# Kernel tuning notes

Hardware: AMD Instinct MI355X
Metric: run time of the kernel (lower is better)

## Reference

```python
import jax, jax.numpy as jnp
import numpy as np

N = 65536   # base nodes
M = 65536   # union local nodes
E = 1048576 # base edges
EL = 1048576 # local edges
K = 131072  # membership entries
F = 128     # in_channels
H = 128     # hidden_dim
L = 2       # num_layers
OUT = 2
ALPHA = 0.9


def setup_inputs() -> dict:
    key = jax.random.key(0)
    ks = jax.random.split(key, 16)
    s = 1.0 / np.sqrt(H)
    return {
        "x": jax.random.normal(ks[0], (N, F), jnp.float32),
        "edge_index": jax.random.randint(ks[1], (2, E), 0, N, jnp.int64 if jax.config.jax_enable_x64 else jnp.int32),
        "edge_weight": jax.random.uniform(ks[2], (E,), jnp.float32),
        "local_x0": jax.random.normal(ks[3], (M, F), jnp.float32),
        "copy2orig": jax.random.randint(ks[4], (M,), 0, N),
        "local_adj_index": jax.random.randint(ks[5], (2, EL), 0, M),
        "local_adj_value": jax.random.uniform(ks[6], (EL,), jnp.float32),
        "memb_idx": jax.random.randint(ks[7], (K,), 0, M),
        "memb_gid": jax.random.randint(ks[8], (K,), 0, 64),
        "B": 64,
        "Wb_in": jax.random.normal(ks[9], (F, H), jnp.float32) * s,
        "bb_in": jnp.zeros((H,), jnp.float32),
        "Wl_in": jax.random.normal(ks[10], (F, H), jnp.float32) * s,
        "bl_in": jnp.zeros((H,), jnp.float32),
        "W_base": jax.random.normal(ks[11], (L, H, H), jnp.float32) * s,
        "b_base": jnp.zeros((L, H), jnp.float32),
        "W_local": jax.random.normal(ks[12], (L, H, H), jnp.float32) * s,
        "b_local": jnp.zeros((L, H), jnp.float32),
        "Wp": jax.random.normal(ks[13], (H, OUT), jnp.float32) * s,
        "bp": jnp.zeros((OUT,), jnp.float32),
    }


def reference(x, edge_index, edge_weight, local_x0, copy2orig, local_adj_index,
              local_adj_value, memb_idx, memb_gid, B, Wb_in, bb_in, Wl_in, bl_in,
              W_base, b_base, W_local, b_local, Wp, bp):
    n = x.shape[0]
    m = local_x0.shape[0]
    # input projections (dropout is identity in eval mode)
    base_x = jax.nn.relu(x @ Wb_in + bb_in)
    local_x = jax.nn.relu(local_x0 @ Wl_in + bl_in)
    src, dst = edge_index[0], edge_index[1]
    lsrc, ldst = local_adj_index[0], local_adj_index[1]
    for l in range(W_base.shape[0]):
        # base graph propagation: normalized-adjacency spmm then linear+relu
        base_agg = jax.ops.segment_sum(base_x[src] * edge_weight[:, None], dst, num_segments=n)
        base_x = jax.nn.relu(base_agg @ W_base[l] + b_base[l])
        # local union-graph propagation + alpha-mix with base features via copy2orig
        local_agg = jax.ops.segment_sum(local_x[lsrc] * local_adj_value[:, None], ldst, num_segments=m)
        mix = ALPHA * local_agg + (1.0 - ALPHA) * base_x[copy2orig]
        local_x = jax.nn.relu(mix @ W_local[l] + b_local[l])
    # scatter-mean pooling by membership (fused sum + count)
    sub = jax.ops.segment_sum(local_x[memb_idx], memb_gid, num_segments=B)
    cnt = jax.ops.segment_sum(jnp.ones((memb_gid.shape[0], 1), local_x.dtype), memb_gid, num_segments=B)
    sub = sub / jnp.maximum(cnt, 1.0)
    return sub @ Wp + bp
```

## Files before the change

### kernel.cpp

```cpp
#include <hip/hip_runtime.h>

typedef __attribute__((ext_vector_type(8))) short bfrag;
typedef __attribute__((ext_vector_type(4))) float ffrag;

__device__ __forceinline__ ushort f2bf(float f) {
    union { float f; unsigned u; } v{f};
    unsigned r = v.u + 0x7fff + ((v.u >> 16) & 1);
    return (ushort)(r >> 16);
}
__device__ __forceinline__ float bf2f(ushort u) {
    union { unsigned u; float f; } v{(unsigned)u << 16};
    return v.f;
}
__device__ __forceinline__ float bflo(unsigned u) {
    union { unsigned u; float f; } v{u << 16};
    return v.f;
}
__device__ __forceinline__ float bfhi(unsigned u) {
    union { unsigned u; float f; } v{u & 0xffff0000u};
    return v.f;
}


__global__ __launch_bounds__(256) void zero_all(int* __restrict__ a, int* __restrict__ b,
                                                int* __restrict__ c, int* __restrict__ d) {
    int i = blockIdx.x * 256 + threadIdx.x;
    if (i < 256) { a[i] = 0; b[i] = 0; }
    if (i < 64) c[i] = 0;
    if (i < 64 * 128) d[i] = 0;
}


__global__ __launch_bounds__(256) void bhist(const int* __restrict__ dst, int* __restrict__ bcount) {
    __shared__ int h[256];
    const int t = threadIdx.x;
    h[t] = 0;
    __syncthreads();
    const int base = blockIdx.x * 4096;
#pragma unroll
    for (int u = 0; u < 16; ++u)
        atomicAdd(&h[((unsigned)dst[base + u * 256 + t]) >> 8], 1);
    __syncthreads();
    atomicAdd(&bcount[t], h[t]);
}

__global__ __launch_bounds__(256) void bscan(const int* __restrict__ bcount, int* __restrict__ bstart,
                                             int* __restrict__ bcursor) {
    __shared__ int s[256];
    const int t = threadIdx.x;
    int c = bcount[t];
    s[t] = c;
    __syncthreads();
    for (int o = 1; o < 256; o <<= 1) {
        int add = (t >= o) ? s[t - o] : 0;
        __syncthreads();
        s[t] += add;
        __syncthreads();
    }
    int excl = s[t] - c;
    bstart[t] = excl;
    bcursor[t] = excl;
    if (t == 255) bstart[256] = s[t];
}

#define CH 4096

__global__ __launch_bounds__(1024) void bucket1(const int* __restrict__ src, const int* __restrict__ dst,
                                                const float* __restrict__ w, int* __restrict__ bcursor,
                                                int2* __restrict__ staged) {
    __shared__ int cnt_s[256], base_l[256], base_g[256], cur[256];
    __shared__ int2 stage[CH];
    __shared__ unsigned char bb[CH];
    const int t = threadIdx.x;
    const int base = blockIdx.x * CH;
    if (t < 256) cnt_s[t] = 0;
    __syncthreads();
#pragma unroll
    for (int u = 0; u < CH / 1024; ++u) {
        int b = ((unsigned)dst[base + u * 1024 + t]) >> 8;
        atomicAdd(&cnt_s[b], 1);
    }
    __syncthreads();
    int v = 0;
    if (t < 256) { v = cnt_s[t]; base_l[t] = v; }
    __syncthreads();
    for (int o = 1; o < 256; o <<= 1) {
        int add = 0;
        if (t < 256 && t >= o) add = base_l[t - o];
        __syncthreads();
        if (t < 256) base_l[t] += add;
        __syncthreads();
    }
    if (t < 256) {
        int excl = base_l[t] - v;
        base_l[t] = excl;
        cur[t] = excl;
        base_g[t] = atomicAdd(&bcursor[t], v);
    }
    __syncthreads();
#pragma unroll
    for (int u = 0; u < CH / 1024; ++u) {
        int e = base + u * 1024 + t;
        int d = dst[e];
        int b = ((unsigned)d) >> 8;
        int p = atomicAdd(&cur[b], 1);
        stage[p] = make_int2((src[e] & 0xffff) | ((d & 255) << 16), __float_as_int(w[e]));
        bb[p] = (unsigned char)b;
    }
    __syncthreads();
    for (int i = t; i < CH; i += 1024) {
        int b = bb[i];
        staged[base_g[b] + (i - base_l[b])] = stage[i];
    }
}

__global__ __launch_bounds__(1024) void bucket2n(const int* __restrict__ bstart, const int2* __restrict__ staged,
                                                 int* __restrict__ start, int2* __restrict__ edges) {
    __shared__ int cnt[256], excl[256], cur[256];
    const int t = threadIdx.x;
    const int b = blockIdx.x;
    if (t < 256) cnt[t] = 0;
    __syncthreads();
    const int s0 = bstart[b];
    const int s1 = bstart[b + 1];
    for (int i = s0 + t; i < s1; i += 1024) {
        int dl = (staged[i].x >> 16) & 0xff;
        atomicAdd(&cnt[dl], 1);
    }
    __syncthreads();
    int v = 0;
    if (t < 256) { v = cnt[t]; excl[t] = v; }
    __syncthreads();
    for (int o = 1; o < 256; o <<= 1) {
        int add = 0;
        if (t < 256 && t >= o) add = excl[t - o];
        __syncthreads();
        if (t < 256) excl[t] += add;
        __syncthreads();
    }
    if (t < 256) {
        int e = excl[t] - v;
        cur[t] = e;
        start[b * 256 + t] = s0 + e;
        if (b == 255 && t == 255) start[256 * 256] = s1;
    }
    __syncthreads();
    for (int i = s0 + t; i < s1; i += 1024) {
        int2 se = staged[i];
        int dl = (se.x >> 16) & 0xff;
        int p = s0 + atomicAdd(&cur[dl], 1);
        edges[p] = make_int2(se.x & 0xffff, se.y);
    }
}


__global__ __launch_bounds__(256) void wprep(const float* __restrict__ Wb_in, const float* __restrict__ Wl_in,
                                             const float* __restrict__ W_base, const float* __restrict__ W_local,
                                             ushort* __restrict__ out) {
    int idx = blockIdx.x * 256 + threadIdx.x;
    int mat = idx >> 14;
    int i = idx & 16383;
    int nn = i >> 7, kk = i & 127;
    const float* src;
    switch (mat) {
        case 0: src = Wb_in; break;
        case 1: src = Wl_in; break;
        case 2: src = W_base; break;
        case 3: src = W_base + 16384; break;
        case 4: src = W_local; break;
        default: src = W_local + 16384; break;
    }
    out[(size_t)mat * 16384 + i] = f2bf(src[kk * 128 + nn]);
}

#define ASTRIDE 136


template <bool A_F32, bool MIX>
__global__ __launch_bounds__(256) void gemm_mfma(const void* __restrict__ Ap, const ushort* __restrict__ A2,
                                                 const int* __restrict__ ridx,
                                                 const ushort* __restrict__ Wt, const float* __restrict__ bias,
                                                 ushort* __restrict__ Y) {
    __shared__ ushort As[64 * ASTRIDE];
    __shared__ ushort Bs[128 * ASTRIDE];
    const int tid = threadIdx.x;
    const int r0 = blockIdx.x * 64;

    if (A_F32) {
        const float* A = (const float*)Ap;
#pragma unroll
        for (int p = 0; p < 8; ++p) {
            int c = p * 256 + tid;
            int row = c >> 5, o4 = (c & 31) * 4;
            float4 v = *(const float4*)(A + (size_t)(r0 + row) * 128 + o4);
            ushort4 u;
            u.x = f2bf(v.x); u.y = f2bf(v.y); u.z = f2bf(v.z); u.w = f2bf(v.w);
            *(ushort4*)&As[row * ASTRIDE + o4] = u;
        }
    } else {
        const ushort* A = (const ushort*)Ap;
#pragma unroll
        for (int p = 0; p < 4; ++p) {
            int c = p * 256 + tid;
            int row = c >> 4, o8 = (c & 15) * 8;
            uint4 v = *(const uint4*)(A + (size_t)(r0 + row) * 128 + o8);
            if (MIX) {
                int rr = ridx[r0 + row];
                uint4 v2 = *(const uint4*)(A2 + (size_t)rr * 128 + o8);
                uint4 o;
                float x0, x1;
                x0 = 0.9f * bflo(v.x) + 0.1f * bflo(v2.x);
                x1 = 0.9f * bfhi(v.x) + 0.1f * bfhi(v2.x);
                o.x = (unsigned)f2bf(x0) | ((unsigned)f2bf(x1) << 16);
                x0 = 0.9f * bflo(v.y) + 0.1f * bflo(v2.y);
                x1 = 0.9f * bfhi(v.y) + 0.1f * bfhi(v2.y);
                o.y = (unsigned)f2bf(x0) | ((unsigned)f2bf(x1) << 16);
                x0 = 0.9f * bflo(v.z) + 0.1f * bflo(v2.z);
                x1 = 0.9f * bfhi(v.z) + 0.1f * bfhi(v2.z);
                o.z = (unsigned)f2bf(x0) | ((unsigned)f2bf(x1) << 16);
                x0 = 0.9f * bflo(v.w) + 0.1f * bflo(v2.w);
                x1 = 0.9f * bfhi(v.w) + 0.1f * bfhi(v2.w);
                o.w = (unsigned)f2bf(x0) | ((unsigned)f2bf(x1) << 16);
                v = o;
            }
            *(uint4*)&As[row * ASTRIDE + o8] = v;
        }
    }
#pragma unroll
    for (int p = 0; p < 8; ++p) {
        int c = p * 256 + tid;
        int n = c >> 4, o8 = (c & 15) * 8;
        *(uint4*)&Bs[n * ASTRIDE + o8] = *(const uint4*)(Wt + n * 128 + o8);
    }
    __syncthreads();

    const int lane = tid & 63;
    const int w = tid >> 6;
    const int wm = (w & 1) * 32;
    const int wn = (w >> 1) * 64;
    const int q = lane >> 4;
    const int l16 = lane & 15;

    ffrag acc[2][4];
#pragma unroll
    for (int mt = 0; mt < 2; ++mt)
#pragma unroll
        for (int nt = 0; nt < 4; ++nt) acc[mt][nt] = (ffrag){0.f, 0.f, 0.f, 0.f};

#pragma unroll
    for (int kc = 0; kc < 4; ++kc) {
        bfrag a[2], b[4];
#pragma unroll
        for (int mt = 0; mt < 2; ++mt)
            a[mt] = *(const bfrag*)&As[(wm + mt * 16 + l16) * ASTRIDE + kc * 32 + q * 8];
#pragma unroll
        for (int nt = 0; nt < 4; ++nt)
            b[nt] = *(const bfrag*)&Bs[(wn + nt * 16 + l16) * ASTRIDE + kc * 32 + q * 8];
#pragma unroll
        for (int mt = 0; mt < 2; ++mt)
#pragma unroll
            for (int nt = 0; nt < 4; ++nt)
                acc[mt][nt] = __builtin_amdgcn_mfma_f32_16x16x32_bf16(a[mt], b[nt], acc[mt][nt], 0, 0, 0);
    }

    float bias_v[4];
#pragma unroll
    for (int nt = 0; nt < 4; ++nt) bias_v[nt] = bias[wn + nt * 16 + l16];
#pragma unroll
    for (int mt = 0; mt < 2; ++mt)
#pragma unroll
        for (int nt = 0; nt < 4; ++nt)
#pragma unroll
            for (int r = 0; r < 4; ++r) {
                int row = r0 + wm + mt * 16 + q * 4 + r;
                int col = wn + nt * 16 + l16;
                float v = fmaxf(acc[mt][nt][r] + bias_v[nt], 0.f);
                Y[(size_t)row * 128 + col] = f2bf(v);
            }
}


__global__ __launch_bounds__(256) void spmm_bf16(const int* __restrict__ start, const int2* __restrict__ edges,
                                                 const ushort* __restrict__ X, ushort* __restrict__ Y, int n) {
    int node = (blockIdx.x * 256 + threadIdx.x) >> 5;
    int lane = threadIdx.x & 31;
    if (node >= n) return;
    int s0 = start[node];
    int s1 = start[node + 1];
    const int f = lane * 4;
    float a0 = 0.f, a1 = 0.f, a2 = 0.f, a3 = 0.f;
    int e = s0;
    for (; e + 4 <= s1; e += 4) {
        int2 e0 = edges[e + 0], e1 = edges[e + 1], e2 = edges[e + 2], e3 = edges[e + 3];
        float w0 = __int_as_float(e0.y), w1 = __int_as_float(e1.y);
        float w2 = __int_as_float(e2.y), w3 = __int_as_float(e3.y);
        ushort4 v0 = *(const ushort4*)(X + (size_t)e0.x * 128 + f);
        ushort4 v1 = *(const ushort4*)(X + (size_t)e1.x * 128 + f);
        ushort4 v2 = *(const ushort4*)(X + (size_t)e2.x * 128 + f);
        ushort4 v3 = *(const ushort4*)(X + (size_t)e3.x * 128 + f);
        a0 += w0 * bf2f(v0.x) + w1 * bf2f(v1.x) + w2 * bf2f(v2.x) + w3 * bf2f(v3.x);
        a1 += w0 * bf2f(v0.y) + w1 * bf2f(v1.y) + w2 * bf2f(v2.y) + w3 * bf2f(v3.y);
        a2 += w0 * bf2f(v0.z) + w1 * bf2f(v1.z) + w2 * bf2f(v2.z) + w3 * bf2f(v3.z);
        a3 += w0 * bf2f(v0.w) + w1 * bf2f(v1.w) + w2 * bf2f(v2.w) + w3 * bf2f(v3.w);
    }
    for (; e < s1; ++e) {
        int2 ee = edges[e];
        float w = __int_as_float(ee.y);
        ushort4 v = *(const ushort4*)(X + (size_t)ee.x * 128 + f);
        a0 += w * bf2f(v.x);
        a1 += w * bf2f(v.y);
        a2 += w * bf2f(v.z);
        a3 += w * bf2f(v.w);
    }
    ushort4 o;
    o.x = f2bf(a0);
    o.y = f2bf(a1);
    o.z = f2bf(a2);
    o.w = f2bf(a3);
    *(ushort4*)(Y + (size_t)node * 128 + f) = o;
}


__global__ __launch_bounds__(256) void pool_hist(const int* __restrict__ memb_gid, int* __restrict__ gcount) {
    __shared__ int h[64];
    int t = threadIdx.x;
    if (t < 64) h[t] = 0;
    __syncthreads();
    int base = blockIdx.x * 1024;
#pragma unroll
    for (int u = 0; u < 4; ++u) atomicAdd(&h[memb_gid[base + u * 256 + t]], 1);
    __syncthreads();
    if (t < 64) atomicAdd(&gcount[t], h[t]);
}

__global__ __launch_bounds__(64) void pool_scan(const int* __restrict__ gcount, int* __restrict__ gstart,
                                                int* __restrict__ cursor) {
    __shared__ int s[64];
    int t = threadIdx.x;
    int c = gcount[t];
    s[t] = c;
    __syncthreads();
    int acc = 0;
    for (int j = 0; j < 64; ++j)
        if (j < t) acc += s[j];
    gstart[t] = acc;
    cursor[t] = acc;
    if (t == 63) gstart[64] = acc + c;
}

__global__ __launch_bounds__(256) void pool_scatter(const int* __restrict__ memb_idx,
                                                    const int* __restrict__ memb_gid,
                                                    int* __restrict__ cursor, int* __restrict__ sorted_idx) {
    __shared__ int lhist[64];
    __shared__ int lbase[64];
    __shared__ int loff[1024];
    int t = threadIdx.x;
    if (t < 64) lhist[t] = 0;
    __syncthreads();
    int base = blockIdx.x * 1024;
    int g[4], ix[4];
#pragma unroll
    for (int u = 0; u < 4; ++u) {
        int e = base + u * 256 + t;
        g[u] = memb_gid[e];
        ix[u] = memb_idx[e];
        loff[u * 256 + t] = atomicAdd(&lhist[g[u]], 1);
    }
    __syncthreads();
    if (t < 64) lbase[t] = atomicAdd(&cursor[t], lhist[t]);
    __syncthreads();
#pragma unroll
    for (int u = 0; u < 4; ++u) {
        int pos = lbase[g[u]] + loff[u * 256 + t];
        sorted_idx[pos] = ix[u];
    }
}

__global__ __launch_bounds__(256) void pool_accum(const int* __restrict__ gstart, const int* __restrict__ sorted_idx,
                                                  const ushort* __restrict__ X, float* __restrict__ gsum) {
    const int g = blockIdx.x >> 5;
    const int sgm = blockIdx.x & 31;
    const int gs = gstart[g];
    const int cnt = gstart[g + 1] - gs;
    const int e_begin = gs + ((cnt * sgm) >> 5);
    const int e_end = gs + ((cnt * (sgm + 1)) >> 5);
    const int t = threadIdx.x;
    const int fp = t & 63;
    const int sub = t >> 6;
    float ax = 0.f, ay = 0.f;
#pragma unroll 4
    for (int e = e_begin + sub; e < e_end; e += 4) {
        int idx = sorted_idx[e];
        ushort2 u = *(const ushort2*)(X + (size_t)idx * 128 + fp * 2);
        ax += bf2f(u.x);
        ay += bf2f(u.y);
    }
    __shared__ float sx[256], sy[256];
    sx[t] = ax;
    sy[t] = ay;
    __syncthreads();
    if (t < 64) {
        atomicAdd(&gsum[g * 128 + fp * 2 + 0], sx[t] + sx[t + 64] + sx[t + 128] + sx[t + 192]);
        atomicAdd(&gsum[g * 128 + fp * 2 + 1], sy[t] + sy[t + 64] + sy[t + 128] + sy[t + 192]);
    }
}


__global__ __launch_bounds__(128) void final_kernel(const float* __restrict__ gsum, const int* __restrict__ gcnt,
                                                    const float* __restrict__ Wp, const float* __restrict__ bp,
                                                    float* __restrict__ out) {
    int t = threadIdx.x;
    int g = t >> 1;
    int o = t & 1;
    float inv = 1.f / fmaxf((float)gcnt[g], 1.f);
    float acc = bp[o];
    for (int f = 0; f < 128; ++f) acc += gsum[g * 128 + f] * inv * Wp[f * 2 + o];
    out[g * 2 + o] = acc;
}


extern "C" void kernel_launch(void* const* d_in, const int* in_sizes, int n_in,
                              void* d_out, int out_size, void* d_ws, size_t ws_size,
                              hipStream_t stream) {
    const float* x              = (const float*)d_in[0];
    const int*   edge_index     = (const int*)d_in[1];
    const float* edge_weight    = (const float*)d_in[2];
    const float* local_x0       = (const float*)d_in[3];
    const int*   copy2orig      = (const int*)d_in[4];
    const int*   local_adj_idx  = (const int*)d_in[5];
    const float* local_adj_val  = (const float*)d_in[6];
    const int*   memb_idx       = (const int*)d_in[7];
    const int*   memb_gid       = (const int*)d_in[8];
    const float* Wb_in          = (const float*)d_in[10];
    const float* bb_in          = (const float*)d_in[11];
    const float* Wl_in          = (const float*)d_in[12];
    const float* bl_in          = (const float*)d_in[13];
    const float* W_base         = (const float*)d_in[14];
    const float* b_base         = (const float*)d_in[15];
    const float* W_local        = (const float*)d_in[16];
    const float* b_local        = (const float*)d_in[17];
    const float* Wp             = (const float*)d_in[18];
    const float* bp             = (const float*)d_in[19];
    float* out = (float*)d_out;

    constexpr int N = 65536, M = 65536, E = 1048576, EL = 1048576, K = 131072, H = 128;

    char* wsb = (char*)d_ws;
    size_t off = 0;
    auto alloc = [&](size_t bytes) -> char* {
        char* p = wsb + off;
        off += (bytes + 255) & ~(size_t)255;
        return p;
    };
    int*    bs_start = (int*)alloc((size_t)(N + 1) * 4);
    int2*   bs_edges = (int2*)alloc((size_t)E * 8);
    int2*   bs_stage = (int2*)alloc((size_t)E * 8);
    int*    bs_bcnt  = (int*)alloc(256 * 4);
    int*    bs_bsta  = (int*)alloc(257 * 4);
    int*    bs_bcur  = (int*)alloc(256 * 4);
    int*    ls_start = (int*)alloc((size_t)(M + 1) * 4);
    int2*   ls_edges = (int2*)alloc((size_t)EL * 8);
    int2*   ls_stage = (int2*)alloc((size_t)EL * 8);
    int*    ls_bcnt  = (int*)alloc(256 * 4);
    int*    ls_bsta  = (int*)alloc(257 * 4);
    int*    ls_bcur  = (int*)alloc(256 * 4);
    ushort* bufA     = (ushort*)alloc((size_t)N * H * 2);
    ushort* bufB     = (ushort*)alloc((size_t)M * H * 2);
    ushort* bufC     = (ushort*)alloc((size_t)N * H * 2);
    ushort* bufD     = (ushort*)alloc((size_t)M * H * 2);
    ushort* wt       = (ushort*)alloc((size_t)6 * 16384 * 2);
    int*    p_gcnt   = (int*)alloc(64 * 4);
    int*    p_gstart = (int*)alloc(65 * 4);
    int*    p_cursor = (int*)alloc(64 * 4);
    int*    p_sorted = (int*)alloc((size_t)K * 4);
    float*  pool_sum = (float*)alloc(64 * 128 * 4);

    const int* b_src = edge_index;
    const int* b_dst = edge_index + E;
    const int* l_src = local_adj_idx;
    const int* l_dst = local_adj_idx + EL;

    zero_all<<<32, 256, 0, stream>>>(bs_bcnt, ls_bcnt, p_gcnt, (int*)pool_sum);

    wprep<<<384, 256, 0, stream>>>(Wb_in, Wl_in, W_base, W_local, wt);

    bhist<<<E / 4096, 256, 0, stream>>>(b_dst, bs_bcnt);
    bscan<<<1, 256, 0, stream>>>(bs_bcnt, bs_bsta, bs_bcur);
    bucket1<<<E / CH, 1024, 0, stream>>>(b_src, b_dst, edge_weight, bs_bcur, bs_stage);
    bucket2n<<<256, 1024, 0, stream>>>(bs_bsta, bs_stage, bs_start, bs_edges);

    bhist<<<EL / 4096, 256, 0, stream>>>(l_dst, ls_bcnt);
    bscan<<<1, 256, 0, stream>>>(ls_bcnt, ls_bsta, ls_bcur);
    bucket1<<<EL / CH, 1024, 0, stream>>>(l_src, l_dst, local_adj_val, ls_bcur, ls_stage);
    bucket2n<<<256, 1024, 0, stream>>>(ls_bsta, ls_stage, ls_start, ls_edges);

    pool_hist<<<K / 1024, 256, 0, stream>>>(memb_gid, p_gcnt);
    pool_scan<<<1, 64, 0, stream>>>(p_gcnt, p_gstart, p_cursor);
    pool_scatter<<<K / 1024, 256, 0, stream>>>(memb_idx, memb_gid, p_cursor, p_sorted);

    gemm_mfma<true, false><<<N / 64, 256, 0, stream>>>(x, nullptr, nullptr, wt, bb_in, bufA);
    gemm_mfma<true, false><<<M / 64, 256, 0, stream>>>(local_x0, nullptr, nullptr, wt + 16384, bl_in, bufB);

    for (int l = 0; l < 2; ++l) {
        spmm_bf16<<<N * 32 / 256, 256, 0, stream>>>(bs_start, bs_edges, bufA, bufC, N);
        spmm_bf16<<<M * 32 / 256, 256, 0, stream>>>(ls_start, ls_edges, bufB, bufD, M);
        gemm_mfma<false, false><<<N / 64, 256, 0, stream>>>(bufC, nullptr, nullptr,
                                                            wt + (size_t)(2 + l) * 16384, b_base + (size_t)l * H, bufA);
        gemm_mfma<false, true><<<M / 64, 256, 0, stream>>>(bufD, bufA, copy2orig,
                                                           wt + (size_t)(4 + l) * 16384, b_local + (size_t)l * H, bufB);
    }

    pool_accum<<<64 * 32, 256, 0, stream>>>(p_gstart, p_sorted, bufB, pool_sum);
    final_kernel<<<1, 128, 0, stream>>>(pool_sum, p_gcnt, Wp, bp, out);
}
```

Baseline: 458.3 us.

## Fuse SpMM aggregation with following MFMA GEMM and alpha-mix per layer

Replaces the separate SpMM and GEMM kernels with one kernel per graph that aggregates 64 node rows into shared memory, then runs the MFMA GEMM with bias and ReLU on that tile. The alpha-mix is now applied in fp32 on the aggregate before the bf16 rounding, rather than on rounded bf16 inputs inside the GEMM. Ping-pong buffers avoid read/write aliasing. This removes the intermediate bf16 writes and reads of the aggregated features and two kernel launches per layer. In exchange the weight fragments are read straight from global memory instead of shared memory, and each block serialises 8 node aggregations before the GEMM, which can lower occupancy and latency hiding.

```diff
diff --git a/kernel.cpp b/kernel.cpp
--- a/kernel.cpp
+++ b/kernel.cpp
@@ -176,9 +176,7 @@
 #define ASTRIDE 136
 
 
-template <bool A_F32, bool MIX>
-__global__ __launch_bounds__(256) void gemm_mfma(const void* __restrict__ Ap, const ushort* __restrict__ A2,
-                                                 const int* __restrict__ ridx,
+__global__ __launch_bounds__(256) void gemm_mfma(const float* __restrict__ A,
                                                  const ushort* __restrict__ Wt, const float* __restrict__ bias,
                                                  ushort* __restrict__ Y) {
     __shared__ ushort As[64 * ASTRIDE];
@@ -186,45 +184,14 @@
     const int tid = threadIdx.x;
     const int r0 = blockIdx.x * 64;
 
-    if (A_F32) {
-        const float* A = (const float*)Ap;
-#pragma unroll
-        for (int p = 0; p < 8; ++p) {
-            int c = p * 256 + tid;
-            int row = c >> 5, o4 = (c & 31) * 4;
-            float4 v = *(const float4*)(A + (size_t)(r0 + row) * 128 + o4);
-            ushort4 u;
-            u.x = f2bf(v.x); u.y = f2bf(v.y); u.z = f2bf(v.z); u.w = f2bf(v.w);
-            *(ushort4*)&As[row * ASTRIDE + o4] = u;
-        }
-    } else {
-        const ushort* A = (const ushort*)Ap;
-#pragma unroll
-        for (int p = 0; p < 4; ++p) {
-            int c = p * 256 + tid;
-            int row = c >> 4, o8 = (c & 15) * 8;
-            uint4 v = *(const uint4*)(A + (size_t)(r0 + row) * 128 + o8);
-            if (MIX) {
-                int rr = ridx[r0 + row];
-                uint4 v2 = *(const uint4*)(A2 + (size_t)rr * 128 + o8);
-                uint4 o;
-                float x0, x1;
-                x0 = 0.9f * bflo(v.x) + 0.1f * bflo(v2.x);
-                x1 = 0.9f * bfhi(v.x) + 0.1f * bfhi(v2.x);
-                o.x = (unsigned)f2bf(x0) | ((unsigned)f2bf(x1) << 16);
-                x0 = 0.9f * bflo(v.y) + 0.1f * bflo(v2.y);
-                x1 = 0.9f * bfhi(v.y) + 0.1f * bfhi(v2.y);
-                o.y = (unsigned)f2bf(x0) | ((unsigned)f2bf(x1) << 16);
-                x0 = 0.9f * bflo(v.z) + 0.1f * bflo(v2.z);
-                x1 = 0.9f * bfhi(v.z) + 0.1f * bfhi(v2.z);
-                o.z = (unsigned)f2bf(x0) | ((unsigned)f2bf(x1) << 16);
-                x0 = 0.9f * bflo(v.w) + 0.1f * bflo(v2.w);
-                x1 = 0.9f * bfhi(v.w) + 0.1f * bfhi(v2.w);
-                o.w = (unsigned)f2bf(x0) | ((unsigned)f2bf(x1) << 16);
-                v = o;
-            }
-            *(uint4*)&As[row * ASTRIDE + o8] = v;
-        }
+#pragma unroll
+    for (int p = 0; p < 8; ++p) {
+        int c = p * 256 + tid;
+        int row = c >> 5, o4 = (c & 31) * 4;
+        float4 v = *(const float4*)(A + (size_t)(r0 + row) * 128 + o4);
+        ushort4 u;
+        u.x = f2bf(v.x); u.y = f2bf(v.y); u.z = f2bf(v.z); u.w = f2bf(v.w);
+        *(ushort4*)&As[row * ASTRIDE + o4] = u;
     }
 #pragma unroll
     for (int p = 0; p < 8; ++p) {
@@ -280,44 +247,107 @@
 }
 
 
-__global__ __launch_bounds__(256) void spmm_bf16(const int* __restrict__ start, const int2* __restrict__ edges,
-                                                 const ushort* __restrict__ X, ushort* __restrict__ Y, int n) {
-    int node = (blockIdx.x * 256 + threadIdx.x) >> 5;
-    int lane = threadIdx.x & 31;
-    if (node >= n) return;
-    int s0 = start[node];
-    int s1 = start[node + 1];
-    const int f = lane * 4;
-    float a0 = 0.f, a1 = 0.f, a2 = 0.f, a3 = 0.f;
-    int e = s0;
-    for (; e + 4 <= s1; e += 4) {
-        int2 e0 = edges[e + 0], e1 = edges[e + 1], e2 = edges[e + 2], e3 = edges[e + 3];
-        float w0 = __int_as_float(e0.y), w1 = __int_as_float(e1.y);
-        float w2 = __int_as_float(e2.y), w3 = __int_as_float(e3.y);
-        ushort4 v0 = *(const ushort4*)(X + (size_t)e0.x * 128 + f);
-        ushort4 v1 = *(const ushort4*)(X + (size_t)e1.x * 128 + f);
-        ushort4 v2 = *(const ushort4*)(X + (size_t)e2.x * 128 + f);
-        ushort4 v3 = *(const ushort4*)(X + (size_t)e3.x * 128 + f);
-        a0 += w0 * bf2f(v0.x) + w1 * bf2f(v1.x) + w2 * bf2f(v2.x) + w3 * bf2f(v3.x);
-        a1 += w0 * bf2f(v0.y) + w1 * bf2f(v1.y) + w2 * bf2f(v2.y) + w3 * bf2f(v3.y);
-        a2 += w0 * bf2f(v0.z) + w1 * bf2f(v1.z) + w2 * bf2f(v2.z) + w3 * bf2f(v3.z);
-        a3 += w0 * bf2f(v0.w) + w1 * bf2f(v1.w) + w2 * bf2f(v2.w) + w3 * bf2f(v3.w);
-    }
-    for (; e < s1; ++e) {
-        int2 ee = edges[e];
-        float w = __int_as_float(ee.y);
-        ushort4 v = *(const ushort4*)(X + (size_t)ee.x * 128 + f);
-        a0 += w * bf2f(v.x);
-        a1 += w * bf2f(v.y);
-        a2 += w * bf2f(v.z);
-        a3 += w * bf2f(v.w);
-    }
-    ushort4 o;
-    o.x = f2bf(a0);
-    o.y = f2bf(a1);
-    o.z = f2bf(a2);
-    o.w = f2bf(a3);
-    *(ushort4*)(Y + (size_t)node * 128 + f) = o;
+template <bool MIX>
+__global__ __launch_bounds__(256) void spmm_gemm(const int* __restrict__ start, const int2* __restrict__ edges,
+                                                 const ushort* __restrict__ X, const ushort* __restrict__ A2,
+                                                 const int* __restrict__ ridx, const ushort* __restrict__ Wt,
+                                                 const float* __restrict__ bias, ushort* __restrict__ Y) {
+    __shared__ ushort As[64 * ASTRIDE];
+    const int tid = threadIdx.x;
+    const int r0 = blockIdx.x * 64;
+    const int hw = tid >> 5;
+    const int lane32 = tid & 31;
+    const int f = lane32 * 4;
+
+    for (int it = 0; it < 8; ++it) {
+        const int nl = it * 8 + hw;
+        const int node = r0 + nl;
+        const int s0 = start[node];
+        const int s1 = start[node + 1];
+        float a0 = 0.f, a1 = 0.f, a2 = 0.f, a3 = 0.f;
+        int e = s0;
+        for (; e + 4 <= s1; e += 4) {
+            int2 e0 = edges[e + 0], e1 = edges[e + 1], e2 = edges[e + 2], e3 = edges[e + 3];
+            float w0 = __int_as_float(e0.y), w1 = __int_as_float(e1.y);
+            float w2 = __int_as_float(e2.y), w3 = __int_as_float(e3.y);
+            ushort4 v0 = *(const ushort4*)(X + (size_t)e0.x * 128 + f);
+            ushort4 v1 = *(const ushort4*)(X + (size_t)e1.x * 128 + f);
+            ushort4 v2 = *(const ushort4*)(X + (size_t)e2.x * 128 + f);
+            ushort4 v3 = *(const ushort4*)(X + (size_t)e3.x * 128 + f);
+            a0 += w0 * bf2f(v0.x) + w1 * bf2f(v1.x) + w2 * bf2f(v2.x) + w3 * bf2f(v3.x);
+            a1 += w0 * bf2f(v0.y) + w1 * bf2f(v1.y) + w2 * bf2f(v2.y) + w3 * bf2f(v3.y);
+            a2 += w0 * bf2f(v0.z) + w1 * bf2f(v1.z) + w2 * bf2f(v2.z) + w3 * bf2f(v3.z);
+            a3 += w0 * bf2f(v0.w) + w1 * bf2f(v1.w) + w2 * bf2f(v2.w) + w3 * bf2f(v3.w);
+        }
+        for (; e < s1; ++e) {
+            int2 ee = edges[e];
+            float w = __int_as_float(ee.y);
+            ushort4 v = *(const ushort4*)(X + (size_t)ee.x * 128 + f);
+            a0 += w * bf2f(v.x);
+            a1 += w * bf2f(v.y);
+            a2 += w * bf2f(v.z);
+            a3 += w * bf2f(v.w);
+        }
+        if (MIX) {
+            int rr = ridx[node];
+            ushort4 v2 = *(const ushort4*)(A2 + (size_t)rr * 128 + f);
+            a0 = 0.9f * a0 + 0.1f * bf2f(v2.x);
+            a1 = 0.9f * a1 + 0.1f * bf2f(v2.y);
+            a2 = 0.9f * a2 + 0.1f * bf2f(v2.z);
+            a3 = 0.9f * a3 + 0.1f * bf2f(v2.w);
+        }
+        ushort4 o;
+        o.x = f2bf(a0);
+        o.y = f2bf(a1);
+        o.z = f2bf(a2);
+        o.w = f2bf(a3);
+        *(ushort4*)&As[nl * ASTRIDE + f] = o;
+    }
+    __syncthreads();
+
+    const int lane = tid & 63;
+    const int w = tid >> 6;
+    const int wm = (w & 1) * 32;
+    const int wn = (w >> 1) * 64;
+    const int q = lane >> 4;
+    const int l16 = lane & 15;
+
+    ffrag acc[2][4];
+#pragma unroll
+    for (int mt = 0; mt < 2; ++mt)
+#pragma unroll
+        for (int nt = 0; nt < 4; ++nt) acc[mt][nt] = (ffrag){0.f, 0.f, 0.f, 0.f};
+
+#pragma unroll
+    for (int kc = 0; kc < 4; ++kc) {
+        bfrag a[2], b[4];
+#pragma unroll
+        for (int mt = 0; mt < 2; ++mt)
+            a[mt] = *(const bfrag*)&As[(wm + mt * 16 + l16) * ASTRIDE + kc * 32 + q * 8];
+#pragma unroll
+        for (int nt = 0; nt < 4; ++nt)
+            b[nt] = *(const bfrag*)(Wt + (size_t)(wn + nt * 16 + l16) * 128 + kc * 32 + q * 8);
+#pragma unroll
+        for (int mt = 0; mt < 2; ++mt)
+#pragma unroll
+            for (int nt = 0; nt < 4; ++nt)
+                acc[mt][nt] = __builtin_amdgcn_mfma_f32_16x16x32_bf16(a[mt], b[nt], acc[mt][nt], 0, 0, 0);
+    }
+
+    float bias_v[4];
+#pragma unroll
+    for (int nt = 0; nt < 4; ++nt) bias_v[nt] = bias[wn + nt * 16 + l16];
+#pragma unroll
+    for (int mt = 0; mt < 2; ++mt)
+#pragma unroll
+        for (int nt = 0; nt < 4; ++nt)
+#pragma unroll
+            for (int r = 0; r < 4; ++r) {
+                int row = r0 + wm + mt * 16 + q * 4 + r;
+                int col = wn + nt * 16 + l16;
+                float v = fmaxf(acc[mt][nt][r] + bias_v[nt], 0.f);
+                Y[(size_t)row * 128 + col] = f2bf(v);
+            }
 }
 
 
@@ -498,16 +528,18 @@
     pool_scan<<<1, 64, 0, stream>>>(p_gcnt, p_gstart, p_cursor);
     pool_scatter<<<K / 1024, 256, 0, stream>>>(memb_idx, memb_gid, p_cursor, p_sorted);
 
-    gemm_mfma<true, false><<<N / 64, 256, 0, stream>>>(x, nullptr, nullptr, wt, bb_in, bufA);
-    gemm_mfma<true, false><<<M / 64, 256, 0, stream>>>(local_x0, nullptr, nullptr, wt + 16384, bl_in, bufB);
+    gemm_mfma<<<N / 64, 256, 0, stream>>>(x, wt, bb_in, bufA);
+    gemm_mfma<<<M / 64, 256, 0, stream>>>(local_x0, wt + 16384, bl_in, bufB);
 
     for (int l = 0; l < 2; ++l) {
-        spmm_bf16<<<N * 32 / 256, 256, 0, stream>>>(bs_start, bs_edges, bufA, bufC, N);
-        spmm_bf16<<<M * 32 / 256, 256, 0, stream>>>(ls_start, ls_edges, bufB, bufD, M);
-        gemm_mfma<false, false><<<N / 64, 256, 0, stream>>>(bufC, nullptr, nullptr,
-                                                            wt + (size_t)(2 + l) * 16384, b_base + (size_t)l * H, bufA);
-        gemm_mfma<false, true><<<M / 64, 256, 0, stream>>>(bufD, bufA, copy2orig,
-                                                           wt + (size_t)(4 + l) * 16384, b_local + (size_t)l * H, bufB);
+        const ushort* Xb = l ? bufC : bufA;
+        ushort*       Yb = l ? bufA : bufC;
+        const ushort* Xl = l ? bufD : bufB;
+        ushort*       Yl = l ? bufB : bufD;
+        spmm_gemm<false><<<N / 64, 256, 0, stream>>>(bs_start, bs_edges, Xb, nullptr, nullptr,
+                                                     wt + (size_t)(2 + l) * 16384, b_base + (size_t)l * H, Yb);
+        spmm_gemm<true><<<M / 64, 256, 0, stream>>>(ls_start, ls_edges, Xl, Yb, copy2orig,
+                                                    wt + (size_t)(4 + l) * 16384, b_local + (size_t)l * H, Yl);
     }
 
     pool_accum<<<64 * 32, 256, 0, stream>>>(p_gstart, p_sorted, bufB, pool_sum);
```

Result: slower. 500.2 us (+9.1%).

## Merge base and local graph kernels into combined launches with 512 buckets

Applied to the files above, without the earlier changes.

Combines the base and local pipelines into shared launches: weight prep with zeroing, histogram, scan, two bucket passes, the input GEMMs and the per-layer SpMMs each become one launch covering both graphs. The coarse bucket count goes from 256 to 512 (128 nodes per bucket) with smaller per-block chunks, so the second-level sort handles fewer nodes per bucket. The aim is to cut launch count and fill the GPU better when each graph alone would leave CUs idle. It adds a branch on block index and more per-block scan work.

```diff
diff --git a/kernel.cpp b/kernel.cpp
--- a/kernel.cpp
+++ b/kernel.cpp
@@ -22,215 +22,216 @@
 }
 
 
-__global__ __launch_bounds__(256) void zero_all(int* __restrict__ a, int* __restrict__ b,
-                                                int* __restrict__ c, int* __restrict__ d) {
-    int i = blockIdx.x * 256 + threadIdx.x;
-    if (i < 256) { a[i] = 0; b[i] = 0; }
-    if (i < 64) c[i] = 0;
-    if (i < 64 * 128) d[i] = 0;
-}
-
-
-__global__ __launch_bounds__(256) void bhist(const int* __restrict__ dst, int* __restrict__ bcount) {
-    __shared__ int h[256];
+__global__ __launch_bounds__(256) void wprep_zero(const float* __restrict__ Wb_in, const float* __restrict__ Wl_in,
+                                                  const float* __restrict__ W_base, const float* __restrict__ W_local,
+                                                  ushort* __restrict__ out,
+                                                  int* __restrict__ z_a, int* __restrict__ z_b,
+                                                  int* __restrict__ z_c, int* __restrict__ z_d) {
+    const int bid = blockIdx.x;
+    const int t = threadIdx.x;
+    if (bid < 384) {
+        int idx = bid * 256 + t;
+        int mat = idx >> 14;
+        int i = idx & 16383;
+        int nn = i >> 7, kk = i & 127;
+        const float* src;
+        switch (mat) {
+            case 0: src = Wb_in; break;
+            case 1: src = Wl_in; break;
+            case 2: src = W_base; break;
+            case 3: src = W_base + 16384; break;
+            case 4: src = W_local; break;
+            default: src = W_local + 16384; break;
+        }
+        out[(size_t)mat * 16384 + i] = f2bf(src[kk * 128 + nn]);
+    } else {
+        int i = (bid - 384) * 256 + t;
+        if (i < 512) { z_a[i] = 0; z_b[i] = 0; }
+        if (i < 64) z_c[i] = 0;
+        z_d[i] = 0;
+    }
+}
+
+
+#define NB 512
+#define BSH 7
+#define CH2 2048
+
+__global__ __launch_bounds__(256) void bhist2(const int* __restrict__ b_dst, const int* __restrict__ l_dst,
+                                              int* __restrict__ b_cnt, int* __restrict__ l_cnt) {
+    __shared__ int h[NB];
     const int t = threadIdx.x;
     h[t] = 0;
-    __syncthreads();
-    const int base = blockIdx.x * 4096;
+    h[t + 256] = 0;
+    __syncthreads();
+    const int g = blockIdx.x >> 8;
+    const int* dst = g ? l_dst : b_dst;
+    int* cnt = g ? l_cnt : b_cnt;
+    const int base = (blockIdx.x & 255) * 4096;
 #pragma unroll
     for (int u = 0; u < 16; ++u)
-        atomicAdd(&h[((unsigned)dst[base + u * 256 + t]) >> 8], 1);
-    __syncthreads();
-    atomicAdd(&bcount[t], h[t]);
-}
-
-__global__ __launch_bounds__(256) void bscan(const int* __restrict__ bcount, int* __restrict__ bstart,
-                                             int* __restrict__ bcursor) {
-    __shared__ int s[256];
+        atomicAdd(&h[((unsigned)dst[base + u * 256 + t]) >> BSH], 1);
+    __syncthreads();
+    atomicAdd(&cnt[t], h[t]);
+    atomicAdd(&cnt[t + 256], h[t + 256]);
+}
+
+__global__ __launch_bounds__(512) void bscan2(const int* __restrict__ b_cnt, int* __restrict__ b_sta, int* __restrict__ b_cur,
+                                              const int* __restrict__ l_cnt, int* __restrict__ l_sta, int* __restrict__ l_cur) {
+    __shared__ int s[NB];
     const int t = threadIdx.x;
-    int c = bcount[t];
+    const int* cnt = blockIdx.x ? l_cnt : b_cnt;
+    int* sta = blockIdx.x ? l_sta : b_sta;
+    int* cur = blockIdx.x ? l_cur : b_cur;
+    int c = cnt[t];
     s[t] = c;
     __syncthreads();
-    for (int o = 1; o < 256; o <<= 1) {
+    for (int o = 1; o < NB; o <<= 1) {
         int add = (t >= o) ? s[t - o] : 0;
         __syncthreads();
         s[t] += add;
         __syncthreads();
     }
-    int excl = s[t] - c;
-    bstart[t] = excl;
-    bcursor[t] = excl;
-    if (t == 255) bstart[256] = s[t];
-}
-
-#define CH 4096
-
-__global__ __launch_bounds__(1024) void bucket1(const int* __restrict__ src, const int* __restrict__ dst,
-                                                const float* __restrict__ w, int* __restrict__ bcursor,
-                                                int2* __restrict__ staged) {
-    __shared__ int cnt_s[256], base_l[256], base_g[256], cur[256];
-    __shared__ int2 stage[CH];
-    __shared__ unsigned char bb[CH];
+    sta[t] = s[t] - c;
+    cur[t] = s[t] - c;
+    if (t == NB - 1) sta[NB] = s[t];
+}
+
+__global__ __launch_bounds__(1024) void bucket1b(const int* __restrict__ b_src, const int* __restrict__ b_dst,
+                                                 const float* __restrict__ b_w, int* __restrict__ b_cur,
+                                                 int2* __restrict__ b_staged,
+                                                 const int* __restrict__ l_src, const int* __restrict__ l_dst,
+                                                 const float* __restrict__ l_w, int* __restrict__ l_cur,
+                                                 int2* __restrict__ l_staged) {
+    __shared__ int cnt_s[NB], base_l[NB], base_g[NB], curs[NB];
+    __shared__ int2 stage[CH2];
+    __shared__ ushort bb[CH2];
     const int t = threadIdx.x;
-    const int base = blockIdx.x * CH;
-    if (t < 256) cnt_s[t] = 0;
-    __syncthreads();
-#pragma unroll
-    for (int u = 0; u < CH / 1024; ++u) {
-        int b = ((unsigned)dst[base + u * 1024 + t]) >> 8;
+    const int g = blockIdx.x >> 9;
+    const int* src = g ? l_src : b_src;
+    const int* dst = g ? l_dst : b_dst;
+    const float* w = g ? l_w : b_w;
+    int* bcursor = g ? l_cur : b_cur;
+    int2* staged = g ? l_staged : b_staged;
+    const int base = (blockIdx.x & 511) * CH2;
+    if (t < NB) cnt_s[t] = 0;
+    __syncthreads();
+#pragma unroll
+    for (int u = 0; u < CH2 / 1024; ++u) {
+        int b = ((unsigned)dst[base + u * 1024 + t]) >> BSH;
         atomicAdd(&cnt_s[b], 1);
     }
     __syncthreads();
     int v = 0;
-    if (t < 256) { v = cnt_s[t]; base_l[t] = v; }
-    __syncthreads();
-    for (int o = 1; o < 256; o <<= 1) {
+    if (t < NB) { v = cnt_s[t]; base_l[t] = v; }
+    __syncthreads();
+    for (int o = 1; o < NB; o <<= 1) {
         int add = 0;
-        if (t < 256 && t >= o) add = base_l[t - o];
+        if (t < NB && t >= o) add = base_l[t - o];
         __syncthreads();
-        if (t < 256) base_l[t] += add;
+        if (t < NB) base_l[t] += add;
         __syncthreads();
     }
-    if (t < 256) {
+    if (t < NB) {
         int excl = base_l[t] - v;
         base_l[t] = excl;
-        cur[t] = excl;
+        curs[t] = excl;
         base_g[t] = atomicAdd(&bcursor[t], v);
     }
     __syncthreads();
 #pragma unroll
-    for (int u = 0; u < CH / 1024; ++u) {
+    for (int u = 0; u < CH2 / 1024; ++u) {
         int e = base + u * 1024 + t;
         int d = dst[e];
-        int b = ((unsigned)d) >> 8;
-        int p = atomicAdd(&cur[b], 1);
-        stage[p] = make_int2((src[e] & 0xffff) | ((d & 255) << 16), __float_as_int(w[e]));
-        bb[p] = (unsigned char)b;
-    }
-    __syncthreads();
-    for (int i = t; i < CH; i += 1024) {
+        int b = ((unsigned)d) >> BSH;
+        int p = atomicAdd(&curs[b], 1);
+        stage[p] = make_int2((src[e] & 0xffff) | ((d & 127) << 16), __float_as_int(w[e]));
+        bb[p] = (ushort)b;
+    }
+    __syncthreads();
+    for (int i = t; i < CH2; i += 1024) {
         int b = bb[i];
         staged[base_g[b] + (i - base_l[b])] = stage[i];
     }
 }
 
-__global__ __launch_bounds__(1024) void bucket2n(const int* __restrict__ bstart, const int2* __restrict__ staged,
-                                                 int* __restrict__ start, int2* __restrict__ edges) {
-    __shared__ int cnt[256], excl[256], cur[256];
+__global__ __launch_bounds__(1024) void bucket2b(const int* __restrict__ b_sta, const int2* __restrict__ b_staged,
+                                                 int* __restrict__ b_start, int2* __restrict__ b_edges,
+                                                 const int* __restrict__ l_sta, const int2* __restrict__ l_staged,
+                                                 int* __restrict__ l_start, int2* __restrict__ l_edges) {
+    __shared__ int cnt[128], excl[128], curs[128];
     const int t = threadIdx.x;
-    const int b = blockIdx.x;
-    if (t < 256) cnt[t] = 0;
-    __syncthreads();
-    const int s0 = bstart[b];
-    const int s1 = bstart[b + 1];
+    const int g = blockIdx.x >> 9;
+    const int b = blockIdx.x & 511;
+    const int* bsta = g ? l_sta : b_sta;
+    const int2* staged = g ? l_staged : b_staged;
+    int* start = g ? l_start : b_start;
+    int2* edges = g ? l_edges : b_edges;
+    if (t < 128) cnt[t] = 0;
+    __syncthreads();
+    const int s0 = bsta[b];
+    const int s1 = bsta[b + 1];
     for (int i = s0 + t; i < s1; i += 1024) {
-        int dl = (staged[i].x >> 16) & 0xff;
+        int dl = (staged[i].x >> 16) & 127;
         atomicAdd(&cnt[dl], 1);
     }
     __syncthreads();
     int v = 0;
-    if (t < 256) { v = cnt[t]; excl[t] = v; }
-    __syncthreads();
-    for (int o = 1; o < 256; o <<= 1) {
+    if (t < 128) { v = cnt[t]; excl[t] = v; }
+    __syncthreads();
+    for (int o = 1; o < 128; o <<= 1) {
         int add = 0;
-        if (t < 256 && t >= o) add = excl[t - o];
+        if (t < 128 && t >= o) add = excl[t - o];
         __syncthreads();
-        if (t < 256) excl[t] += add;
+        if (t < 128) excl[t] += add;
         __syncthreads();
     }
-    if (t < 256) {
+    if (t < 128) {
         int e = excl[t] - v;
-        cur[t] = e;
-        start[b * 256 + t] = s0 + e;
-        if (b == 255 && t == 255) start[256 * 256] = s1;
+        curs[t] = e;
+        start[b * 128 + t] = s0 + e;
+        if (b == 511 && t == 127) start[65536] = s1;
     }
     __syncthreads();
     for (int i = s0 + t; i < s1; i += 1024) {
         int2 se = staged[i];
-        int dl = (se.x >> 16) & 0xff;
-        int p = s0 + atomicAdd(&cur[dl], 1);
+        int dl = (se.x >> 16) & 127;
+        int p = s0 + atomicAdd(&curs[dl], 1);
         edges[p] = make_int2(se.x & 0xffff, se.y);
     }
 }
 
-
-__global__ __launch_bounds__(256) void wprep(const float* __restrict__ Wb_in, const float* __restrict__ Wl_in,
-                                             const float* __restrict__ W_base, const float* __restrict__ W_local,
-                                             ushort* __restrict__ out) {
-    int idx = blockIdx.x * 256 + threadIdx.x;
-    int mat = idx >> 14;
-    int i = idx & 16383;
-    int nn = i >> 7, kk = i & 127;
-    const float* src;
-    switch (mat) {
-        case 0: src = Wb_in; break;
-        case 1: src = Wl_in; break;
-        case 2: src = W_base; break;
-        case 3: src = W_base + 16384; break;
-        case 4: src = W_local; break;
-        default: src = W_local + 16384; break;
-    }
-    out[(size_t)mat * 16384 + i] = f2bf(src[kk * 128 + nn]);
-}
-
 #define ASTRIDE 136
 
 
-template <bool A_F32, bool MIX>
-__global__ __launch_bounds__(256) void gemm_mfma(const void* __restrict__ Ap, const ushort* __restrict__ A2,
-                                                 const int* __restrict__ ridx,
-                                                 const ushort* __restrict__ Wt, const float* __restrict__ bias,
-                                                 ushort* __restrict__ Y) {
+__global__ __launch_bounds__(256) void gemm_in2(const float* __restrict__ Ab, const float* __restrict__ Al,
+                                                const ushort* __restrict__ Wt,
+                                                const float* __restrict__ biasb, const float* __restrict__ biasl,
+                                                ushort* __restrict__ Yb, ushort* __restrict__ Yl) {
     __shared__ ushort As[64 * ASTRIDE];
     __shared__ ushort Bs[128 * ASTRIDE];
     const int tid = threadIdx.x;
-    const int r0 = blockIdx.x * 64;
-
-    if (A_F32) {
-        const float* A = (const float*)Ap;
-#pragma unroll
-        for (int p = 0; p < 8; ++p) {
-            int c = p * 256 + tid;
-            int row = c >> 5, o4 = (c & 31) * 4;
-            float4 v = *(const float4*)(A + (size_t)(r0 + row) * 128 + o4);
-            ushort4 u;
-            u.x = f2bf(v.x); u.y = f2bf(v.y); u.z = f2bf(v.z); u.w = f2bf(v.w);
-            *(ushort4*)&As[row * ASTRIDE + o4] = u;
-        }
-    } else {
-        const ushort* A = (const ushort*)Ap;
-#pragma unroll
-        for (int p = 0; p < 4; ++p) {
-            int c = p * 256 + tid;
-            int row = c >> 4, o8 = (c & 15) * 8;
-            uint4 v = *(const uint4*)(A + (size_t)(r0 + row) * 128 + o8);
-            if (MIX) {
-                int rr = ridx[r0 + row];
-                uint4 v2 = *(const uint4*)(A2 + (size_t)rr * 128 + o8);
-                uint4 o;
-                float x0, x1;
-                x0 = 0.9f * bflo(v.x) + 0.1f * bflo(v2.x);
-                x1 = 0.9f * bfhi(v.x) + 0.1f * bfhi(v2.x);
-                o.x = (unsigned)f2bf(x0) | ((unsigned)f2bf(x1) << 16);
-                x0 = 0.9f * bflo(v.y) + 0.1f * bflo(v2.y);
-                x1 = 0.9f * bfhi(v.y) + 0.1f * bfhi(v2.y);
-                o.y = (unsigned)f2bf(x0) | ((unsigned)f2bf(x1) << 16);
-                x0 = 0.9f * bflo(v.z) + 0.1f * bflo(v2.z);
-                x1 = 0.9f * bfhi(v.z) + 0.1f * bfhi(v2.z);
-                o.z = (unsigned)f2bf(x0) | ((unsigned)f2bf(x1) << 16);
-                x0 = 0.9f * bflo(v.w) + 0.1f * bflo(v2.w);
-                x1 = 0.9f * bfhi(v.w) + 0.1f * bfhi(v2.w);
-                o.w = (unsigned)f2bf(x0) | ((unsigned)f2bf(x1) << 16);
-                v = o;
-            }
-            *(uint4*)&As[row * ASTRIDE + o8] = v;
-        }
+    const int g = blockIdx.x >> 10;
+    const float* A = g ? Al : Ab;
+    const ushort* W = Wt + (size_t)g * 16384;
+    const float* bias = g ? biasl : biasb;
+    ushort* Y = g ? Yl : Yb;
+    const int r0 = (blockIdx.x & 1023) * 64;
+
+#pragma unroll
+    for (int p = 0; p < 8; ++p) {
+        int c = p * 256 + tid;
+        int row = c >> 5, o4 = (c & 31) * 4;
+        float4 v = *(const float4*)(A + (size_t)(r0 + row) * 128 + o4);
+        ushort4 u;
+        u.x = f2bf(v.x); u.y = f2bf(v.y); u.z = f2bf(v.z); u.w = f2bf(v.w);
+        *(ushort4*)&As[row * ASTRIDE + o4] = u;
     }
 #pragma unroll
     for (int p = 0; p < 8; ++p) {
         int c = p * 256 + tid;
         int n = c >> 4, o8 = (c & 15) * 8;
-        *(uint4*)&Bs[n * ASTRIDE + o8] = *(const uint4*)(Wt + n * 128 + o8);
+        *(uint4*)&Bs[n * ASTRIDE + o8] = *(const uint4*)(W + n * 128 + o8);
     }
     __syncthreads();
 
@@ -280,11 +281,107 @@
 }
 
 
-__global__ __launch_bounds__(256) void spmm_bf16(const int* __restrict__ start, const int2* __restrict__ edges,
-                                                 const ushort* __restrict__ X, ushort* __restrict__ Y, int n) {
-    int node = (blockIdx.x * 256 + threadIdx.x) >> 5;
+template <bool MIX>
+__global__ __launch_bounds__(256) void gemm_layer(const ushort* __restrict__ A, const ushort* __restrict__ A2,
+                                                  const int* __restrict__ ridx,
+                                                  const ushort* __restrict__ Wt, const float* __restrict__ bias,
+                                                  ushort* __restrict__ Y) {
+    __shared__ ushort As[64 * ASTRIDE];
+    __shared__ ushort Bs[128 * ASTRIDE];
+    const int tid = threadIdx.x;
+    const int r0 = blockIdx.x * 64;
+
+#pragma unroll
+    for (int p = 0; p < 4; ++p) {
+        int c = p * 256 + tid;
+        int row = c >> 4, o8 = (c & 15) * 8;
+        uint4 v = *(const uint4*)(A + (size_t)(r0 + row) * 128 + o8);
+        if (MIX) {
+            int rr = ridx[r0 + row];
+            uint4 v2 = *(const uint4*)(A2 + (size_t)rr * 128 + o8);
+            uint4 o;
+            float x0, x1;
+            x0 = 0.9f * bflo(v.x) + 0.1f * bflo(v2.x);
+            x1 = 0.9f * bfhi(v.x) + 0.1f * bfhi(v2.x);
+            o.x = (unsigned)f2bf(x0) | ((unsigned)f2bf(x1) << 16);
+            x0 = 0.9f * bflo(v.y) + 0.1f * bflo(v2.y);
+            x1 = 0.9f * bfhi(v.y) + 0.1f * bfhi(v2.y);
+            o.y = (unsigned)f2bf(x0) | ((unsigned)f2bf(x1) << 16);
+            x0 = 0.9f * bflo(v.z) + 0.1f * bflo(v2.z);
+            x1 = 0.9f * bfhi(v.z) + 0.1f * bfhi(v2.z);
+            o.z = (unsigned)f2bf(x0) | ((unsigned)f2bf(x1) << 16);
+            x0 = 0.9f * bflo(v.w) + 0.1f * bflo(v2.w);
+            x1 = 0.9f * bfhi(v.w) + 0.1f * bfhi(v2.w);
+            o.w = (unsigned)f2bf(x0) | ((unsigned)f2bf(x1) << 16);
+            v = o;
+        }
+        *(uint4*)&As[row * ASTRIDE + o8] = v;
+    }
+#pragma unroll
+    for (int p = 0; p < 8; ++p) {
+        int c = p * 256 + tid;
+        int n = c >> 4, o8 = (c & 15) * 8;
+        *(uint4*)&Bs[n * ASTRIDE + o8] = *(const uint4*)(Wt + n * 128 + o8);
+    }
+    __syncthreads();
+
+    const int lane = tid & 63;
+    const int w = tid >> 6;
+    const int wm = (w & 1) * 32;
+    const int wn = (w >> 1) * 64;
+    const int q = lane >> 4;
+    const int l16 = lane & 15;
+
+    ffrag acc[2][4];
+#pragma unroll
+    for (int mt = 0; mt < 2; ++mt)
+#pragma unroll
+        for (int nt = 0; nt < 4; ++nt) acc[mt][nt] = (ffrag){0.f, 0.f, 0.f, 0.f};
+
+#pragma unroll
+    for (int kc = 0; kc < 4; ++kc) {
+        bfrag a[2], b[4];
+#pragma unroll
+        for (int mt = 0; mt < 2; ++mt)
+            a[mt] = *(const bfrag*)&As[(wm + mt * 16 + l16) * ASTRIDE + kc * 32 + q * 8];
+#pragma unroll
+        for (int nt = 0; nt < 4; ++nt)
+            b[nt] = *(const bfrag*)&Bs[(wn + nt * 16 + l16) * ASTRIDE + kc * 32 + q * 8];
+#pragma unroll
+        for (int mt = 0; mt < 2; ++mt)
+#pragma unroll
+            for (int nt = 0; nt < 4; ++nt)
+                acc[mt][nt] = __builtin_amdgcn_mfma_f32_16x16x32_bf16(a[mt], b[nt], acc[mt][nt], 0, 0, 0);
+    }
+
+    float bias_v[4];
+#pragma unroll
+    for (int nt = 0; nt < 4; ++nt) bias_v[nt] = bias[wn + nt * 16 + l16];
+#pragma unroll
+    for (int mt = 0; mt < 2; ++mt)
+#pragma unroll
+        for (int nt = 0; nt < 4; ++nt)
+#pragma unroll
+            for (int r = 0; r < 4; ++r) {
+                int row = r0 + wm + mt * 16 + q * 4 + r;
+                int col = wn + nt * 16 + l16;
+                float v = fmaxf(acc[mt][nt][r] + bias_v[nt], 0.f);
+                Y[(size_t)row * 128 + col] = f2bf(v);
+            }
+}
+
+
+__global__ __launch_bounds__(256) void spmm2(const int* __restrict__ bs_start, const int2* __restrict__ bs_edges,
+                                             const ushort* __restrict__ Xb, ushort* __restrict__ Yb,
+                                             const int* __restrict__ ls_start, const int2* __restrict__ ls_edges,
+                                             const ushort* __restrict__ Xl, ushort* __restrict__ Yl) {
+    const int g = blockIdx.x >> 13;
+    const int* start = g ? ls_start : bs_start;
+    const int2* edges = g ? ls_edges : bs_edges;
+    const ushort* X = g ? Xl : Xb;
+    ushort* Y = g ? Yl : Yb;
+    int node = (((blockIdx.x & 8191) * 256) + threadIdx.x) >> 5;
     int lane = threadIdx.x & 31;
-    if (node >= n) return;
     int s0 = start[node];
     int s1 = start[node + 1];
     const int f = lane * 4;
@@ -455,15 +552,15 @@
     int*    bs_start = (int*)alloc((size_t)(N + 1) * 4);
     int2*   bs_edges = (int2*)alloc((size_t)E * 8);
     int2*   bs_stage = (int2*)alloc((size_t)E * 8);
-    int*    bs_bcnt  = (int*)alloc(256 * 4);
-    int*    bs_bsta  = (int*)alloc(257 * 4);
-    int*    bs_bcur  = (int*)alloc(256 * 4);
+    int*    bs_bcnt  = (int*)alloc(NB * 4);
+    int*    bs_bsta  = (int*)alloc((NB + 1) * 4);
+    int*    bs_bcur  = (int*)alloc(NB * 4);
     int*    ls_start = (int*)alloc((size_t)(M + 1) * 4);
     int2*   ls_edges = (int2*)alloc((size_t)EL * 8);
     int2*   ls_stage = (int2*)alloc((size_t)EL * 8);
-    int*    ls_bcnt  = (int*)alloc(256 * 4);
-    int*    ls_bsta  = (int*)alloc(257 * 4);
-    int*    ls_bcur  = (int*)alloc(256 * 4);
+    int*    ls_bcnt  = (int*)alloc(NB * 4);
+    int*    ls_bsta  = (int*)alloc((NB + 1) * 4);
+    int*    ls_bcur  = (int*)alloc(NB * 4);
     ushort* bufA     = (ushort*)alloc((size_t)N * H * 2);
     ushort* bufB     = (ushort*)alloc((size_t)M * H * 2);
     ushort* bufC     = (ushort*)alloc((size_t)N * H * 2);
@@ -480,34 +577,29 @@
     const int* l_src = local_adj_idx;
     const int* l_dst = local_adj_idx + EL;
 
-    zero_all<<<32, 256, 0, stream>>>(bs_bcnt, ls_bcnt, p_gcnt, (int*)pool_sum);
-
-    wprep<<<384, 256, 0, stream>>>(Wb_in, Wl_in, W_base, W_local, wt);
-
-    bhist<<<E / 4096, 256, 0, stream>>>(b_dst, bs_bcnt);
-    bscan<<<1, 256, 0, stream>>>(bs_bcnt, bs_bsta, bs_bcur);
-    bucket1<<<E / CH, 1024, 0, stream>>>(b_src, b_dst, edge_weight, bs_bcur, bs_stage);
-    bucket2n<<<256, 1024, 0, stream>>>(bs_bsta, bs_stage, bs_start, bs_edges);
-
-    bhist<<<EL / 4096, 256, 0, stream>>>(l_dst, ls_bcnt);
-    bscan<<<1, 256, 0, stream>>>(ls_bcnt, ls_bsta, ls_bcur);
-    bucket1<<<EL / CH, 1024, 0, stream>>>(l_src, l_dst, local_adj_val, ls_bcur, ls_stage);
-    bucket2n<<<256, 1024, 0, stream>>>(ls_bsta, ls_stage, ls_start, ls_edges);
+    wprep_zero<<<416, 256, 0, stream>>>(Wb_in, Wl_in, W_base, W_local, wt,
+                                        bs_bcnt, ls_bcnt, p_gcnt, (int*)pool_sum);
+
+    bhist2<<<512, 256, 0, stream>>>(b_dst, l_dst, bs_bcnt, ls_bcnt);
+    bscan2<<<2, 512, 0, stream>>>(bs_bcnt, bs_bsta, bs_bcur, ls_bcnt, ls_bsta, ls_bcur);
+    bucket1b<<<1024, 1024, 0, stream>>>(b_src, b_dst, edge_weight, bs_bcur, bs_stage,
+                                        l_src, l_dst, local_adj_val, ls_bcur, ls_stage);
+    bucket2b<<<1024, 1024, 0, stream>>>(bs_bsta, bs_stage, bs_start, bs_edges,
+                                        ls_bsta, ls_stage, ls_start, ls_edges);
 
     pool_hist<<<K / 1024, 256, 0, stream>>>(memb_gid, p_gcnt);
     pool_scan<<<1, 64, 0, stream>>>(p_gcnt, p_gstart, p_cursor);
     pool_scatter<<<K / 1024, 256, 0, stream>>>(memb_idx, memb_gid, p_cursor, p_sorted);
 
-    gemm_mfma<true, false><<<N / 64, 256, 0, stream>>>(x, nullptr, nullptr, wt, bb_in, bufA);
-    gemm_mfma<true, false><<<M / 64, 256, 0, stream>>>(local_x0, nullptr, nullptr, wt + 16384, bl_in, bufB);
+    gemm_in2<<<2048, 256, 0, stream>>>(x, local_x0, wt, bb_in, bl_in, bufA, bufB);
 
     for (int l = 0; l < 2; ++l) {
-        spmm_bf16<<<N * 32 / 256, 256, 0, stream>>>(bs_start, bs_edges, bufA, bufC, N);
-        spmm_bf16<<<M * 32 / 256, 256, 0, stream>>>(ls_start, ls_edges, bufB, bufD, M);
-        gemm_mfma<false, false><<<N / 64, 256, 0, stream>>>(bufC, nullptr, nullptr,
-                                                            wt + (size_t)(2 + l) * 16384, b_base + (size_t)l * H, bufA);
-        gemm_mfma<false, true><<<M / 64, 256, 0, stream>>>(bufD, bufA, copy2orig,
-                                                           wt + (size_t)(4 + l) * 16384, b_local + (size_t)l * H, bufB);
+        spmm2<<<16384, 256, 0, stream>>>(bs_start, bs_edges, bufA, bufC,
+                                         ls_start, ls_edges, bufB, bufD);
+        gemm_layer<false><<<N / 64, 256, 0, stream>>>(bufC, nullptr, nullptr,
+                                                      wt + (size_t)(2 + l) * 16384, b_base + (size_t)l * H, bufA);
+        gemm_layer<true><<<M / 64, 256, 0, stream>>>(bufD, bufA, copy2orig,
+                                                     wt + (size_t)(4 + l) * 16384, b_local + (size_t)l * H, bufB);
     }
 
     pool_accum<<<64 * 32, 256, 0, stream>>>(p_gstart, p_sorted, bufB, pool_sum);
```

Measured after the change: 429.4 us. 1.07x faster.
